# Kernel optimization log

Hardware: AMD Instinct MI355X
Metric: run time of the kernel (lower is better)

## Reference

```python
import jax, jax.numpy as jnp
import numpy as np

M, K, N = 8000, 120, 8000
CHUNK_ROW, CHUNK_COL = 128, 64
# padded dims per the module's __init__ arithmetic
M_PAD = (CHUNK_ROW - M % CHUNK_ROW) % CHUNK_ROW + M   # 8064
K_PAD = (CHUNK_COL - K % CHUNK_COL) % CHUNK_COL + K   # 128
N_PAD = (CHUNK_ROW - N % CHUNK_ROW) % CHUNK_ROW + N   # 8064


def setup_inputs() -> dict:
    key = jax.random.key(0)
    kA, kB, kb = jax.random.split(key, 3)
    A = jax.random.normal(kA, (M, K), dtype=jnp.float32)
    Bm = jax.random.normal(kB, (K, N), dtype=jnp.float32)
    bias = jax.random.normal(kb, (N,), dtype=jnp.float32)
    return {"A": A, "Bm": Bm, "bias": bias}


def reference(A, Bm, bias):
    # Zero-pad A to [M_PAD, K_PAD] and B to [K_PAD, N_PAD]; the original
    # blocked loop over (chunk_row, chunk_col) tiles with psum accumulation
    # is mathematically a single dense GEMM on the padded operands.
    A_p = jnp.pad(A, ((0, M_PAD - A.shape[0]), (0, K_PAD - A.shape[1])))
    B_p = jnp.pad(Bm, ((0, K_PAD - Bm.shape[0]), (0, N_PAD - Bm.shape[1])))
    gemm = A_p @ B_p                      # [M_PAD, N_PAD]
    nb = bias.shape[0]
    # bias.shape[0] (=N) != padded N -> add to first nb cols then slice
    gemm = gemm.at[:, :nb].add(bias)
    return gemm[:, :nb]                   # [M_PAD, N]
```

## Files before the change

kernel.cpp:

```cpp
#include <hip/hip_runtime.h>
#include <hip/hip_bf16.h>
#include <stdint.h>

#define M_DIM 8000
#define K_DIM 120
#define N_DIM 8000
#define M_PADD 8064
#define K_PADD 128

typedef __attribute__((ext_vector_type(8))) __bf16 bf16x8;
typedef __attribute__((ext_vector_type(4))) float f32x4;
typedef __attribute__((ext_vector_type(8))) unsigned short u16x8;

__device__ __forceinline__ unsigned short f2bf(float f) {
  unsigned int u = __builtin_bit_cast(unsigned int, f);
  u += 0x7FFFu + ((u >> 16) & 1u);
  return (unsigned short)(u >> 16);
}

#define CONV_BLOCKS_PER_SIDE 504

__global__ __launch_bounds__(256) void conv_ab_kernel(const float* __restrict__ A,
                                                      const float* __restrict__ B,
                                                      unsigned short* __restrict__ Abf,
                                                      unsigned short* __restrict__ Bbf) {
  const int bid = blockIdx.x;
  if (bid < CONV_BLOCKS_PER_SIDE) {
    int t = bid * 256 + threadIdx.x;
    int row = t >> 4;
    int kg  = t & 15;
    u16x8 v = (u16x8)0;
    if (row < M_DIM && kg < 15) {
      const float* src = A + (size_t)row * K_DIM + kg * 8;
      float4 f0 = *(const float4*)(src);
      float4 f1 = *(const float4*)(src + 4);
      v[0] = f2bf(f0.x); v[1] = f2bf(f0.y); v[2] = f2bf(f0.z); v[3] = f2bf(f0.w);
      v[4] = f2bf(f1.x); v[5] = f2bf(f1.y); v[6] = f2bf(f1.z); v[7] = f2bf(f1.w);
    }
    int off = (kg * 16) ^ ((row & 7) << 4);
    *(u16x8*)((char*)Abf + (size_t)row * 256 + off) = v;
  } else {
    int t = (bid - CONV_BLOCKS_PER_SIDE) * 256 + threadIdx.x;
    int kg = t / M_PADD;
    int n  = t % M_PADD;
    u16x8 v = (u16x8)0;
    if (n < N_DIM && kg < 15) {
      const float* src = B + (size_t)(kg * 8) * N_DIM + n;
#pragma unroll
      for (int j = 0; j < 8; ++j) v[j] = f2bf(src[(size_t)j * N_DIM]);
    }
    int off = (kg * 16) ^ ((n & 7) << 4);
    *(u16x8*)((char*)Bbf + (size_t)n * 256 + off) = v;
  }
}

__global__ __launch_bounds__(512) void gemm_bias_kernel(const unsigned short* __restrict__ Abf,
                                                        const unsigned short* __restrict__ Bbf,
                                                        const float* __restrict__ bias,
                                                        float* __restrict__ out) {
  __shared__ __align__(16) char smem[65536];
  const int bn = blockIdx.x;
  const int bm = blockIdx.y;
  const int tid  = threadIdx.x;
  const int lane = tid & 63;
  const int wave = tid >> 6;
  const int wr = wave >> 2;
  const int wc = wave & 3;

  const char* gA = (const char*)Abf + (size_t)bm * 32768;
  const char* gB = (const char*)Bbf + (size_t)bn * 32768;
#pragma unroll
  for (int i = 0; i < 4; ++i) {
    int off = i * 8192 + tid * 16;
    __builtin_amdgcn_global_load_lds(
        (const __attribute__((address_space(1))) void*)(gA + off),
        (__attribute__((address_space(3))) void*)(smem + off), 16, 0, 0);
    __builtin_amdgcn_global_load_lds(
        (const __attribute__((address_space(1))) void*)(gB + off),
        (__attribute__((address_space(3))) void*)(smem + 32768 + off), 16, 0, 0);
  }
  __syncthreads();

  f32x4 acc[4][2] = {};
  const int l15 = lane & 15;
  const int kq  = lane >> 4;
#pragma unroll
  for (int ks = 0; ks < 4; ++ks) {
    const int kb = (ks * 32 + kq * 8) * 2;
    bf16x8 a[4], b[2];
#pragma unroll
    for (int m = 0; m < 4; ++m) {
      int row = wr * 64 + m * 16 + l15;
      a[m] = *(const bf16x8*)(smem + (size_t)row * 256 + (kb ^ ((row & 7) << 4)));
    }
#pragma unroll
    for (int n = 0; n < 2; ++n) {
      int row = wc * 32 + n * 16 + l15;
      b[n] = *(const bf16x8*)(smem + 32768 + (size_t)row * 256 + (kb ^ ((row & 7) << 4)));
    }
#pragma unroll
    for (int m = 0; m < 4; ++m)
#pragma unroll
      for (int n = 0; n < 2; ++n)
        acc[m][n] = __builtin_amdgcn_mfma_f32_16x16x32_bf16(a[m], b[n], acc[m][n], 0, 0, 0);
  }

  float bv[2];
#pragma unroll
  for (int n = 0; n < 2; ++n) {
    int gcol = bn * 128 + wc * 32 + n * 16 + l15;
    bv[n] = (gcol < N_DIM) ? bias[gcol] : 0.f;
  }

  float* tbuf = (float*)smem;
#pragma unroll
  for (int h = 0; h < 2; ++h) {
    __syncthreads();
    if (wr == h) {
#pragma unroll
      for (int m = 0; m < 4; ++m)
#pragma unroll
        for (int n = 0; n < 2; ++n)
#pragma unroll
          for (int r = 0; r < 4; ++r) {
            int rl = m * 16 + kq * 4 + r;
            int c  = wc * 32 + n * 16 + l15;
            tbuf[rl * 132 + c] = acc[m][n][r] + bv[n];
          }
    }
    __syncthreads();
#pragma unroll
    for (int j = 0; j < 4; ++j) {
      int rl = (wave * 4 + j) * 2 + (lane >> 5);
      int c  = lane & 31;
      f32x4 v = *(const f32x4*)(tbuf + rl * 132 + c * 4);
      int gcol = bn * 128 + c * 4;
      if (gcol < N_DIM) {
        size_t off = (size_t)(bm * 128 + h * 64 + rl) * N_DIM + gcol;
        __builtin_nontemporal_store(v, (f32x4*)(out + off));
      }
    }
  }
}

__global__ __launch_bounds__(256) void fallback_kernel(const float* __restrict__ A,
                                                       const float* __restrict__ B,
                                                       const float* __restrict__ bias,
                                                       float* __restrict__ out) {
  size_t idx = (size_t)blockIdx.x * 256 + threadIdx.x;
  if (idx >= (size_t)M_PADD * N_DIM) return;
  int col = (int)(idx % N_DIM);
  int row = (int)(idx / N_DIM);
  float s = 0.f;
  if (row < M_DIM) {
    for (int k = 0; k < K_DIM; ++k)
      s += A[(size_t)row * K_DIM + k] * B[(size_t)k * N_DIM + col];
  }
  out[idx] = s + bias[col];
}

extern "C" void kernel_launch(void* const* d_in, const int* in_sizes, int n_in,
                              void* d_out, int out_size, void* d_ws, size_t ws_size,
                              hipStream_t stream) {
  const float* A    = (const float*)d_in[0];
  const float* Bm   = (const float*)d_in[1];
  const float* bias = (const float*)d_in[2];
  float* out = (float*)d_out;

  const size_t abf_elems = (size_t)M_PADD * K_PADD;
  const size_t need = abf_elems * 2 * sizeof(unsigned short);
  if (ws_size < need) {
    size_t total = (size_t)M_PADD * N_DIM;
    fallback_kernel<<<dim3((unsigned)((total + 255) / 256)), dim3(256), 0, stream>>>(A, Bm, bias, out);
    return;
  }

  unsigned short* Abf = (unsigned short*)d_ws;
  unsigned short* Bbf = Abf + abf_elems;

  conv_ab_kernel<<<dim3(2 * CONV_BLOCKS_PER_SIDE), dim3(256), 0, stream>>>(A, Bm, Abf, Bbf);
  gemm_bias_kernel<<<dim3(63, 63), dim3(512), 0, stream>>>(Abf, Bbf, bias, out);
}
```

Measured before the change: 58.66 us.

## Reshape GEMM tile to 64x256 with single-pass epilogue and padded B

Changes the block tile from 128x128 to 64x256, so each block loads 16KB of A and 64KB of B into LDS, and B is padded to 8192 columns. The grid becomes 32x126. The epilogue stages the whole tile through LDS in one pass with one pair of barriers instead of two halves, so full 1KB row segments are stored per wave. Launch bounds hint 4 blocks per CU, but the 80KB LDS per block may limit residency. The wider tile also wastes more compute on the padded columns past 8000.

```diff
diff --git a/kernel.cpp b/kernel.cpp
--- a/kernel.cpp
+++ b/kernel.cpp
@@ -6,6 +6,7 @@
 #define K_DIM 120
 #define N_DIM 8000
 #define M_PADD 8064
+#define N_PADB 8192
 #define K_PADD 128
 
 typedef __attribute__((ext_vector_type(8))) __bf16 bf16x8;
@@ -18,14 +19,15 @@
   return (unsigned short)(u >> 16);
 }
 
-#define CONV_BLOCKS_PER_SIDE 504
+#define CONV_A_BLOCKS 504
+#define CONV_B_BLOCKS 512
 
 __global__ __launch_bounds__(256) void conv_ab_kernel(const float* __restrict__ A,
                                                       const float* __restrict__ B,
                                                       unsigned short* __restrict__ Abf,
                                                       unsigned short* __restrict__ Bbf) {
   const int bid = blockIdx.x;
-  if (bid < CONV_BLOCKS_PER_SIDE) {
+  if (bid < CONV_A_BLOCKS) {
     int t = bid * 256 + threadIdx.x;
     int row = t >> 4;
     int kg  = t & 15;
@@ -40,9 +42,9 @@
     int off = (kg * 16) ^ ((row & 7) << 4);
     *(u16x8*)((char*)Abf + (size_t)row * 256 + off) = v;
   } else {
-    int t = (bid - CONV_BLOCKS_PER_SIDE) * 256 + threadIdx.x;
-    int kg = t / M_PADD;
-    int n  = t % M_PADD;
+    int t = (bid - CONV_A_BLOCKS) * 256 + threadIdx.x;
+    int kg = t / N_PADB;
+    int n  = t % N_PADB;
     u16x8 v = (u16x8)0;
     if (n < N_DIM && kg < 15) {
       const float* src = B + (size_t)(kg * 8) * N_DIM + n;
@@ -54,30 +56,32 @@
   }
 }
 
-__global__ __launch_bounds__(512) void gemm_bias_kernel(const unsigned short* __restrict__ Abf,
-                                                        const unsigned short* __restrict__ Bbf,
-                                                        const float* __restrict__ bias,
-                                                        float* __restrict__ out) {
-  __shared__ __align__(16) char smem[65536];
+__global__ __launch_bounds__(512, 4) void gemm_bias_kernel(const unsigned short* __restrict__ Abf,
+                                                           const unsigned short* __restrict__ Bbf,
+                                                           const float* __restrict__ bias,
+                                                           float* __restrict__ out) {
+  __shared__ __align__(16) char smem[81920];
   const int bn = blockIdx.x;
   const int bm = blockIdx.y;
   const int tid  = threadIdx.x;
   const int lane = tid & 63;
   const int wave = tid >> 6;
-  const int wr = wave >> 2;
-  const int wc = wave & 3;
 
-  const char* gA = (const char*)Abf + (size_t)bm * 32768;
-  const char* gB = (const char*)Bbf + (size_t)bn * 32768;
+  const char* gA = (const char*)Abf + (size_t)bm * 16384;
+  const char* gB = (const char*)Bbf + (size_t)bn * 65536;
 #pragma unroll
-  for (int i = 0; i < 4; ++i) {
+  for (int i = 0; i < 2; ++i) {
     int off = i * 8192 + tid * 16;
     __builtin_amdgcn_global_load_lds(
         (const __attribute__((address_space(1))) void*)(gA + off),
         (__attribute__((address_space(3))) void*)(smem + off), 16, 0, 0);
+  }
+#pragma unroll
+  for (int i = 0; i < 8; ++i) {
+    int off = i * 8192 + tid * 16;
     __builtin_amdgcn_global_load_lds(
         (const __attribute__((address_space(1))) void*)(gB + off),
-        (__attribute__((address_space(3))) void*)(smem + 32768 + off), 16, 0, 0);
+        (__attribute__((address_space(3))) void*)(smem + 16384 + off), 16, 0, 0);
   }
   __syncthreads();
 
@@ -90,13 +94,13 @@
     bf16x8 a[4], b[2];
 #pragma unroll
     for (int m = 0; m < 4; ++m) {
-      int row = wr * 64 + m * 16 + l15;
+      int row = m * 16 + l15;
       a[m] = *(const bf16x8*)(smem + (size_t)row * 256 + (kb ^ ((row & 7) << 4)));
     }
 #pragma unroll
     for (int n = 0; n < 2; ++n) {
-      int row = wc * 32 + n * 16 + l15;
-      b[n] = *(const bf16x8*)(smem + 32768 + (size_t)row * 256 + (kb ^ ((row & 7) << 4)));
+      int row = wave * 32 + n * 16 + l15;
+      b[n] = *(const bf16x8*)(smem + 16384 + (size_t)row * 256 + (kb ^ ((row & 7) << 4)));
     }
 #pragma unroll
     for (int m = 0; m < 4; ++m)
@@ -108,37 +112,33 @@
   float bv[2];
 #pragma unroll
   for (int n = 0; n < 2; ++n) {
-    int gcol = bn * 128 + wc * 32 + n * 16 + l15;
+    int gcol = bn * 256 + wave * 32 + n * 16 + l15;
     bv[n] = (gcol < N_DIM) ? bias[gcol] : 0.f;
   }
 
   float* tbuf = (float*)smem;
+  __syncthreads();
 #pragma unroll
-  for (int h = 0; h < 2; ++h) {
-    __syncthreads();
-    if (wr == h) {
+  for (int m = 0; m < 4; ++m)
 #pragma unroll
-      for (int m = 0; m < 4; ++m)
+    for (int n = 0; n < 2; ++n)
 #pragma unroll
-        for (int n = 0; n < 2; ++n)
+      for (int r = 0; r < 4; ++r) {
+        int rl = m * 16 + kq * 4 + r;
+        int c  = wave * 32 + n * 16 + l15;
+        tbuf[rl * 260 + c] = acc[m][n][r] + bv[n];
+      }
+  __syncthreads();
+
+  const int gcol0 = bn * 256 + lane * 4;
+  const bool colok = (gcol0 < N_DIM);
 #pragma unroll
-          for (int r = 0; r < 4; ++r) {
-            int rl = m * 16 + kq * 4 + r;
-            int c  = wc * 32 + n * 16 + l15;
-            tbuf[rl * 132 + c] = acc[m][n][r] + bv[n];
-          }
-    }
-    __syncthreads();
-#pragma unroll
-    for (int j = 0; j < 4; ++j) {
-      int rl = (wave * 4 + j) * 2 + (lane >> 5);
-      int c  = lane & 31;
-      f32x4 v = *(const f32x4*)(tbuf + rl * 132 + c * 4);
-      int gcol = bn * 128 + c * 4;
-      if (gcol < N_DIM) {
-        size_t off = (size_t)(bm * 128 + h * 64 + rl) * N_DIM + gcol;
-        __builtin_nontemporal_store(v, (f32x4*)(out + off));
-      }
+  for (int j = 0; j < 8; ++j) {
+    int row = j * 8 + wave;
+    f32x4 v = *(const f32x4*)(tbuf + row * 260 + lane * 4);
+    if (colok) {
+      size_t off = (size_t)(bm * 64 + row) * N_DIM + gcol0;
+      __builtin_nontemporal_store(v, (f32x4*)(out + off));
     }
   }
 }
@@ -168,7 +168,8 @@
   float* out = (float*)d_out;
 
   const size_t abf_elems = (size_t)M_PADD * K_PADD;
-  const size_t need = abf_elems * 2 * sizeof(unsigned short);
+  const size_t bbf_elems = (size_t)N_PADB * K_PADD;
+  const size_t need = (abf_elems + bbf_elems) * sizeof(unsigned short);
   if (ws_size < need) {
     size_t total = (size_t)M_PADD * N_DIM;
     fallback_kernel<<<dim3((unsigned)((total + 255) / 256)), dim3(256), 0, stream>>>(A, Bm, bias, out);
@@ -178,6 +179,6 @@
   unsigned short* Abf = (unsigned short*)d_ws;
   unsigned short* Bbf = Abf + abf_elems;
 
-  conv_ab_kernel<<<dim3(2 * CONV_BLOCKS_PER_SIDE), dim3(256), 0, stream>>>(A, Bm, Abf, Bbf);
-  gemm_bias_kernel<<<dim3(63, 63), dim3(512), 0, stream>>>(Abf, Bbf, bias, out);
+  conv_ab_kernel<<<dim3(CONV_A_BLOCKS + CONV_B_BLOCKS), dim3(256), 0, stream>>>(A, Bm, Abf, Bbf);
+  gemm_bias_kernel<<<dim3(32, 126), dim3(512), 0, stream>>>(Abf, Bbf, bias, out);
 }
```

New measurement: 57.38 us. 1.02x faster.
